# Kernel tuning notes

Measured on AMD Instinct MI355X. Metric: run time of the kernel, lower is better.

Reference implementation:

```python
import jax, jax.numpy as jnp
import numpy as np

QUERY_DIM = 1024
HIDDEN_DIM = 1024


def setup_inputs() -> dict:
    key = jax.random.key(0)
    k1, k2, k3, k4 = jax.random.split(key, 4)
    query = jax.random.normal(k1, (8, 2048, QUERY_DIM), dtype=jnp.float32)
    info = jax.random.normal(k2, (8, 2048, HIDDEN_DIM), dtype=jnp.float32)
    # nn.Linear params: weight [out, in], bias [out]
    bound = 1.0 / np.sqrt(QUERY_DIM)
    W = jax.random.uniform(k3, (HIDDEN_DIM, QUERY_DIM), jnp.float32, -bound, bound)
    b = jax.random.uniform(k4, (HIDDEN_DIM,), jnp.float32, -bound, bound)
    return {"query": query, "info": info, "W": W, "b": b}


def reference(query, info, W, b):
    # Eval mode: dropout is identity.
    # projected query: [B, S, hidden]
    q = jnp.einsum("bsq,hq->bsh", query, W) + b
    # unscaled attention scores over info rows: [B, S, M]
    scores = jax.nn.softmax(jnp.einsum("bsh,bmh->bsm", q, info), axis=-1)
    # weighted sum of info: [B, S, hidden]
    return jnp.einsum("bsm,bmh->bsh", scores, info)
```

## Files before the change

### kernel.cpp

```cpp
#include <hip/hip_runtime.h>

#define DEVI __device__ __forceinline__

typedef __attribute__((ext_vector_type(4))) float f32x4;
typedef __attribute__((ext_vector_type(8))) short bf16x8;

typedef const unsigned __attribute__((address_space(1))) as1_u32;
typedef unsigned __attribute__((address_space(3))) as3_u32;

DEVI unsigned fbits(float x){ union{float f;unsigned u;} v; v.f=x; return v.u; }
DEVI float bitsf(unsigned u){ union{unsigned u;float f;} v; v.u=u; return v.f; }
DEVI short bf_rne(float x){ unsigned u=fbits(x); u += 0x7fffu + ((u>>16)&1u); return (short)(u>>16); }

DEVI unsigned pack_hi2(unsigned u0, unsigned u1){
#if __has_builtin(__builtin_amdgcn_perm)
  return __builtin_amdgcn_perm(u1, u0, 0x07060302u);
#else
  return (u0 >> 16) | (u1 & 0xffff0000u);
#endif
}
DEVI unsigned pack_rne2(float a, float b){
  return (unsigned)(unsigned short)bf_rne(a) | ((unsigned)(unsigned short)bf_rne(b) << 16);
}

DEVI void gload16(const short* g, short* s){
  __builtin_amdgcn_global_load_lds((as1_u32*)g, (as3_u32*)s, 16, 0, 0);
}

__global__ __launch_bounds__(256)
void k_split(const float* __restrict__ in, short* __restrict__ hi,
             short* __restrict__ lo, const long n4)
{
  long i = (long)blockIdx.x*256 + threadIdx.x;
  const long stride = (long)gridDim.x*256;
  for (; i < n4; i += stride){
    const float4 v = ((const float4*)in)[i];
    const unsigned u0=fbits(v.x), u1=fbits(v.y), u2=fbits(v.z), u3=fbits(v.w);
    ((uint2*)hi)[i] = make_uint2(pack_hi2(u0,u1), pack_hi2(u2,u3));
    const float l0 = v.x - bitsf(u0 & 0xffff0000u);
    const float l1 = v.y - bitsf(u1 & 0xffff0000u);
    const float l2 = v.z - bitsf(u2 & 0xffff0000u);
    const float l3 = v.w - bitsf(u3 & 0xffff0000u);
    ((uint2*)lo)[i] = make_uint2(pack_rne2(l0,l1), pack_rne2(l2,l3));
  }
}

template<int NPHASE, bool BIAS, bool SPLIT_OUT>
__global__ __launch_bounds__(256, 2)
void k_gemm(const short* __restrict__ Ah, const short* __restrict__ Al,
            const short* __restrict__ Bh, const short* __restrict__ Bl,
            void* __restrict__ Cv, const float* __restrict__ bias,
            const int K, const int lda, const int ldb, const int ldc,
            const long sAz, const long sBz, const long sCz, const int loOff)
{
  __shared__ short As[128*64];
  __shared__ short Bs[128*64];

  const int tid = threadIdx.x;
  const int w = tid >> 6, l = tid & 63;
  const long bz = blockIdx.z;
  const size_t aOff = (size_t)bz*sAz + (size_t)blockIdx.x*128*lda;
  const size_t bOff = (size_t)bz*sBz + (size_t)blockIdx.y*128*ldb;

  int srow[4], scol[4];
  short *sA[4], *sB[4];
#pragma unroll
  for (int i = 0; i < 4; ++i){
    const int c = w*4 + i;
    const int r = c*8 + (l>>3);
    srow[i] = r;
    scol[i] = ((l&7) ^ (r&7)) << 3;
    sA[i] = As + c*512;
    sB[i] = Bs + c*512;
  }

  const int wr = w >> 1, wc = w & 1;
  const int fr = l & 15, h4 = l >> 4;

  int aoffs[2][4], boffs[2][4];
#pragma unroll
  for (int kk = 0; kk < 2; ++kk)
#pragma unroll
    for (int m = 0; m < 4; ++m){
      const int ra = wr*64 + m*16 + fr;
      aoffs[kk][m] = ra*64 + (((kk*4 + h4) ^ (ra&7)) << 3);
      const int rb = wc*64 + m*16 + fr;
      boffs[kk][m] = rb*64 + (((kk*4 + h4) ^ (rb&7)) << 3);
    }

  f32x4 acc[4][4];
#pragma unroll
  for (int m = 0; m < 4; ++m)
#pragma unroll
    for (int n = 0; n < 4; ++n){ acc[m][n][0]=0.f; acc[m][n][1]=0.f; acc[m][n][2]=0.f; acc[m][n][3]=0.f; }

#pragma unroll 1
  for (int p = 0; p < NPHASE; ++p){
    const short* Ap = ((NPHASE==3 && p==1) ? Al : Ah) + aOff;
    const short* Bp = ((NPHASE==3 && p==2) ? Bl : Bh) + bOff;
#pragma unroll 1
    for (int kt = 0; kt < K; kt += 64){
#pragma unroll
      for (int i = 0; i < 4; ++i){
        gload16(Ap + (size_t)srow[i]*lda + kt + scol[i], sA[i]);
        gload16(Bp + (size_t)srow[i]*ldb + kt + scol[i], sB[i]);
      }
      __syncthreads();
#pragma unroll
      for (int kk = 0; kk < 2; ++kk){
        bf16x8 bfr[4];
#pragma unroll
        for (int n = 0; n < 4; ++n) bfr[n] = *(const bf16x8*)(Bs + boffs[kk][n]);
#pragma unroll
        for (int m = 0; m < 4; ++m){
          const bf16x8 afr = *(const bf16x8*)(As + aoffs[kk][m]);
#pragma unroll
          for (int n = 0; n < 4; ++n)
            acc[m][n] = __builtin_amdgcn_mfma_f32_16x16x32_bf16(afr, bfr[n], acc[m][n], 0,0,0);
        }
      }
      __syncthreads();
    }
  }

  const int rr = h4*4;
  if constexpr (SPLIT_OUT){
    short* Ch = (short*)Cv + (size_t)bz*sCz
              + (size_t)(blockIdx.x*128 + wr*64)*ldc + blockIdx.y*128 + wc*64;
    short* Cl = Ch + loOff;
#pragma unroll
    for (int n = 0; n < 4; ++n){
      const int col = n*16 + fr;
      const float bv = BIAS ? bias[blockIdx.y*128 + wc*64 + col] : 0.f;
#pragma unroll
      for (int m = 0; m < 4; ++m)
#pragma unroll
        for (int j = 0; j < 4; ++j){
          const float v = acc[m][n][j] + bv;
          const unsigned uh = fbits(v) & 0xffff0000u;
          const size_t idx = (size_t)(m*16 + rr + j)*ldc + col;
          Ch[idx] = (short)(uh >> 16);
          Cl[idx] = bf_rne(v - bitsf(uh));
        }
    }
  } else {
    float* C = (float*)Cv + (size_t)bz*sCz
             + (size_t)(blockIdx.x*128 + wr*64)*ldc + blockIdx.y*128 + wc*64;
#pragma unroll
    for (int n = 0; n < 4; ++n){
      const int col = n*16 + fr;
      const float bv = BIAS ? bias[blockIdx.y*128 + wc*64 + col] : 0.f;
#pragma unroll
      for (int m = 0; m < 4; ++m)
#pragma unroll
        for (int j = 0; j < 4; ++j)
          C[(size_t)(m*16 + rr + j)*ldc + col] = acc[m][n][j] + bv;
    }
  }
}

__global__ __launch_bounds__(256)
void k_transpose_bf16(const float* __restrict__ V, short* __restrict__ T,
                      const int MM, const int DD, const long sVz, const long sTz)
{
  __shared__ float t[64][65];
  const float* Vb = V + (long)blockIdx.z*sVz;
  short* Tb = T + (long)blockIdx.z*sTz;
  const int m0 = blockIdx.x*64, d0 = blockIdx.y*64;
  const int tid = threadIdx.x;
#pragma unroll
  for (int i = 0; i < 4; ++i){
    const int c = tid + 256*i;
    const int r = c >> 4, c4 = (c & 15) * 4;
    const float4 v = *(const float4*)(Vb + (size_t)(m0 + r)*DD + d0 + c4);
    t[r][c4+0] = v.x; t[r][c4+1] = v.y; t[r][c4+2] = v.z; t[r][c4+3] = v.w;
  }
  __syncthreads();
#pragma unroll
  for (int i = 0; i < 4; ++i){
    const int c = tid + 256*i;
    const int d = c >> 4, m4 = (c & 15) * 4;
    short4 o;
    o.x = bf_rne(t[m4+0][d]); o.y = bf_rne(t[m4+1][d]);
    o.z = bf_rne(t[m4+2][d]); o.w = bf_rne(t[m4+3][d]);
    *(short4*)(Tb + (size_t)(d0 + d)*MM + m0 + m4) = o;
  }
}

__global__ __launch_bounds__(256)
void k_softmax_rows(float* __restrict__ Sb, const long sz)
{
  float* row = Sb + (long)blockIdx.y*sz + (long)blockIdx.x*2048;
  short* prow = (short*)row;
  const int tid = threadIdx.x;
  const int lane = tid & 63, wid = tid >> 6;

  const float4 v0 = *(const float4*)(row + tid*4);
  const float4 v1 = *(const float4*)(row + 1024 + tid*4);
  float x[8] = {v0.x, v0.y, v0.z, v0.w, v1.x, v1.y, v1.z, v1.w};

  float mx = x[0];
#pragma unroll
  for (int j = 1; j < 8; ++j) mx = fmaxf(mx, x[j]);
#pragma unroll
  for (int off = 32; off; off >>= 1) mx = fmaxf(mx, __shfl_xor(mx, off));

  __shared__ float red[8];
  if (lane == 0) red[wid] = mx;
  __syncthreads();
  mx = fmaxf(fmaxf(red[0], red[1]), fmaxf(red[2], red[3]));

  float e[8]; float s = 0.f;
#pragma unroll
  for (int j = 0; j < 8; ++j){ e[j] = __expf(x[j] - mx); s += e[j]; }
#pragma unroll
  for (int off = 32; off; off >>= 1) s += __shfl_xor(s, off);
  if (lane == 0) red[4 + wid] = s;
  __syncthreads();
  s = (red[4] + red[5]) + (red[6] + red[7]);
  const float inv = 1.0f / s;

  *(uint2*)(prow + tid*4)        = make_uint2(pack_rne2(e[0]*inv, e[1]*inv), pack_rne2(e[2]*inv, e[3]*inv));
  *(uint2*)(prow + 1024 + tid*4) = make_uint2(pack_rne2(e[4]*inv, e[5]*inv), pack_rne2(e[6]*inv, e[7]*inv));
}

extern "C" void kernel_launch(void* const* d_in, const int* in_sizes, int n_in,
                              void* d_out, int out_size, void* d_ws, size_t ws_size,
                              hipStream_t stream)
{
  const float* query = (const float*)d_in[0];
  const float* info  = (const float*)d_in[1];
  const float* Wm    = (const float*)d_in[2];
  const float* bias  = (const float*)d_in[3];
  float* out = (float*)d_out;

  const int B = 8, S = 2048, M = 2048, D = 1024;
  const size_t PB = (size_t)S * D;

  short* info_hi = (short*)d_ws;
  short* info_lo = info_hi + 16777216;
  short* infoT   = info_lo + 16777216;
  short* W_hi    = infoT   + 16777216;
  short* W_lo    = W_hi    + 1048576;
  float* Sbuf    = (float*)(W_lo + 1048576);
  const size_t sb = (size_t)S * M * sizeof(float);
  size_t avail = ws_size > 104857600ull ? ws_size - 104857600ull : 0;
  int nchunk = (int)(avail / sb); if (nchunk > 8) nchunk = 8; if (nchunk < 1) nchunk = 1;

  short* q_s = (short*)d_out;
  const long qBz = 2*(long)PB;
  const int  qLo = (int)PB;

  k_split<<<1024, 256, 0, stream>>>(Wm, W_hi, W_lo, (long)(D*D/4));

  int nb = 2*nchunk; if (nb > 8) nb = 8;
  for (int q0 = 0; q0 < B; q0 += nb){
    const int cur = (q0 + nb <= B) ? nb : (B - q0);
    short* qt_hi = (short*)Sbuf;
    short* qt_lo = qt_hi + (size_t)cur*PB;
    k_split<<<2048, 256, 0, stream>>>(query + (size_t)q0*PB, qt_hi, qt_lo,
                                      (long)((size_t)cur*PB/4));
    k_gemm<3, true, true><<<dim3(S/128, D/128, cur), 256, 0, stream>>>(
        qt_hi, qt_lo, W_hi, W_lo, q_s + (size_t)q0*qBz, bias,
        D, D, D, D, (long)PB, 0L, qBz, qLo);
  }

  k_split<<<2048, 256, 0, stream>>>(info, info_hi, info_lo, (long)(B*PB/4));
  k_transpose_bf16<<<dim3(M/64, D/64, B), 256, 0, stream>>>(
      info, infoT, M, D, (long)PB, (long)PB);

  for (int b0 = 0; b0 < B; b0 += nchunk){
    const int cur = (b0 + nchunk <= B) ? nchunk : (B - b0);

    const short* qh = q_s + (size_t)b0*qBz;
    k_gemm<3, false, false><<<dim3(S/128, M/128, cur), 256, 0, stream>>>(
        qh, qh + qLo, info_hi + (size_t)b0*PB, info_lo + (size_t)b0*PB,
        Sbuf, nullptr, D, D, D, M, qBz, (long)PB, (long)S*M, 0);

    k_softmax_rows<<<dim3(S, cur), 256, 0, stream>>>(Sbuf, (long)S*M);

    k_gemm<1, false, false><<<dim3(S/128, D/128, cur), 256, 0, stream>>>(
        (const short*)Sbuf, nullptr, infoT + (size_t)b0*PB, nullptr,
        out + (size_t)b0*PB, nullptr, M, 2*M, M, D,
        (long)(2*(size_t)S*M), (long)PB, (long)PB, 0);
  }
}
```

Baseline: 538.0 us.

## Rewrite GEMM as 256x256 double-buffered pipelined tile and fuse info prep

The bf16 MFMA GEMM moves from a 128x128 tile with 256 threads and synchronous single-buffer loads to a 256x256 tile with 512 threads. It double-buffers in 128KB of LDS, interleaves global-to-LDS prefetch with MFMA phases using explicit waitcnt, sched barriers and setprio, and swizzles the workgroup order for L2 locality. The info split and the transpose are fused into one kernel so info is read once. The larger tile raises data reuse and hides load latency, at the cost of heavy register pressure (128 accumulators per lane), fewer workgroups and fragile hand-tuned waitcnt ordering.

```diff
diff --git a/kernel.cpp b/kernel.cpp
--- a/kernel.cpp
+++ b/kernel.cpp
@@ -26,6 +26,16 @@
 DEVI void gload16(const short* g, short* s){
   __builtin_amdgcn_global_load_lds((as1_u32*)g, (as3_u32*)s, 16, 0, 0);
 }
+
+#define SBAR() { __builtin_amdgcn_sched_barrier(0); asm volatile("" ::: "memory"); \
+                 __builtin_amdgcn_s_barrier(); __builtin_amdgcn_sched_barrier(0); }
+
+#define MF(a,b,c) __builtin_amdgcn_mfma_f32_16x16x32_bf16(a,b,c,0,0,0)
+#define MROW(M, x) \
+  acc[M][0] = MF(x, bb0, acc[M][0]); \
+  acc[M][1] = MF(x, bb1, acc[M][1]); \
+  acc[M][2] = MF(x, bb2, acc[M][2]); \
+  acc[M][3] = MF(x, bb3, acc[M][3]);
 
 __global__ __launch_bounds__(256)
 void k_split(const float* __restrict__ in, short* __restrict__ hi,
@@ -46,94 +56,168 @@
 }
 
 template<int NPHASE, bool BIAS, bool SPLIT_OUT>
-__global__ __launch_bounds__(256, 2)
+__global__ __launch_bounds__(512, 2)
 void k_gemm(const short* __restrict__ Ah, const short* __restrict__ Al,
             const short* __restrict__ Bh, const short* __restrict__ Bl,
             void* __restrict__ Cv, const float* __restrict__ bias,
             const int K, const int lda, const int ldb, const int ldc,
             const long sAz, const long sBz, const long sCz, const int loOff)
 {
-  __shared__ short As[128*64];
-  __shared__ short Bs[128*64];
+  __shared__ short LDS[65536];
 
   const int tid = threadIdx.x;
   const int w = tid >> 6, l = tid & 63;
+  const int wr = w >> 2, wc = w & 3;
+  const int fr = l & 15, h4 = l >> 4;
   const long bz = blockIdx.z;
-  const size_t aOff = (size_t)bz*sAz + (size_t)blockIdx.x*128*lda;
-  const size_t bOff = (size_t)bz*sBz + (size_t)blockIdx.y*128*ldb;
-
-  int srow[4], scol[4];
-  short *sA[4], *sB[4];
-#pragma unroll
-  for (int i = 0; i < 4; ++i){
-    const int c = w*4 + i;
-    const int r = c*8 + (l>>3);
-    srow[i] = r;
-    scol[i] = ((l&7) ^ (r&7)) << 3;
-    sA[i] = As + c*512;
-    sB[i] = Bs + c*512;
-  }
-
-  const int wr = w >> 1, wc = w & 1;
-  const int fr = l & 15, h4 = l >> 4;
-
-  int aoffs[2][4], boffs[2][4];
-#pragma unroll
-  for (int kk = 0; kk < 2; ++kk)
-#pragma unroll
-    for (int m = 0; m < 4; ++m){
-      const int ra = wr*64 + m*16 + fr;
-      aoffs[kk][m] = ra*64 + (((kk*4 + h4) ^ (ra&7)) << 3);
-      const int rb = wc*64 + m*16 + fr;
-      boffs[kk][m] = rb*64 + (((kk*4 + h4) ^ (rb&7)) << 3);
-    }
-
-  f32x4 acc[4][4];
-#pragma unroll
-  for (int m = 0; m < 4; ++m)
+
+  const int nwg = gridDim.x * gridDim.y;
+  const int xy  = blockIdx.y * gridDim.x + blockIdx.x;
+  const int q8  = nwg >> 3;
+  const int sw  = (xy & 7) * q8 + (xy >> 3);
+  const int bx  = sw % gridDim.x;
+  const int by  = sw / gridDim.x;
+
+  const size_t aOff = (size_t)bz*sAz + (size_t)bx*256*lda;
+  const size_t bOff = (size_t)bz*sBz + (size_t)by*256*ldb;
+
+  const int sch = (((l & 7) ^ ((l >> 3) & 7)) << 3);
+  const int rA0 = wr*128 + (w & 3)*8 + (l >> 3);
+  int aoffg[4];
+#pragma unroll
+  for (int q2 = 0; q2 < 4; ++q2) aoffg[q2] = (rA0 + 32*q2)*lda;
+  const int rB0 = wc*64 + (w >> 2)*8 + (l >> 3);
+  int boffg[4];
+#pragma unroll
+  for (int j2 = 0; j2 < 4; ++j2) boffg[j2] = (rB0 + 16*j2)*ldb;
+  const int dAu = wr*8192 + (w & 3)*512;
+  const int dBu = 16384 + wc*4096 + (w >> 2)*512;
+
+  const int rbA = (wr*128 + fr)*64;
+  const int rbB = 16384 + (wc*64 + fr)*64;
+  const int c08 = ((h4     ) ^ (l & 7)) << 3;
+  const int c18 = ((h4 + 4 ) ^ (l & 7)) << 3;
+
+  f32x4 acc[8][4];
+#pragma unroll
+  for (int m = 0; m < 8; ++m)
 #pragma unroll
     for (int n = 0; n < 4; ++n){ acc[m][n][0]=0.f; acc[m][n][1]=0.f; acc[m][n][2]=0.f; acc[m][n][3]=0.f; }
 
+  const short* Asrc = Ah + aOff + sch;
+  const short* Bsrc = Bh + bOff + sch;
+  int skt = 0, spass = 0;
+  const int nkt = NPHASE * (K >> 6);
+
+  {
+    short* dB0 = LDS + dBu;
+    short* dA0 = LDS + dAu;
+    gload16(Bsrc + boffg[0], dB0);
+    gload16(Bsrc + boffg[1], dB0 + 1024);
+    gload16(Bsrc + boffg[2], dB0 + 2048);
+    gload16(Bsrc + boffg[3], dB0 + 3072);
+    gload16(Asrc + aoffg[0], dA0);
+    gload16(Asrc + aoffg[1], dA0 + 2048);
+    gload16(Asrc + aoffg[2], dA0 + 4096);
+    gload16(Asrc + aoffg[3], dA0 + 6144);
+  }
+  skt = 64; Asrc += 64; Bsrc += 64;
+  asm volatile("s_waitcnt vmcnt(2)" ::: "memory");
+  SBAR();
+
+#define ADVANCE()                                                            \
+  { skt += 64;                                                               \
+    if (skt == K){ skt = 0; ++spass;                                         \
+      Asrc = ((NPHASE==3 && spass==1) ? Al : Ah) + aOff + sch;               \
+      Bsrc = ((NPHASE==3 && spass==2) ? Bl : Bh) + bOff + sch;               \
+    } else { Asrc += 64; Bsrc += 64; } }
+
+#define TILE(CO, PF, VA, VB)                                                 \
+{                                                                            \
+  const short* pA = LDS + (CO) + rbA;                                        \
+  const short* pB = LDS + (CO) + rbB;                                        \
+  short* dAp = LDS + ((CO)^32768) + dAu;                                     \
+  short* dBp = LDS + ((CO)^32768) + dBu;                                     \
+  bf16x8 aA,aB,aC,aD, bb0,bb1,bb2,bb3;                                       \
+                                            \
+  if (PF){ gload16(Bsrc + boffg[0], dBp); gload16(Bsrc + boffg[1], dBp + 1024); } \
+  bb0 = *(const bf16x8*)(pB +        c08);                                   \
+  bb1 = *(const bf16x8*)(pB + 1024 + c08);                                   \
+  bb2 = *(const bf16x8*)(pB + 2048 + c08);                                   \
+  bb3 = *(const bf16x8*)(pB + 3072 + c08);                                   \
+  aA  = *(const bf16x8*)(pA +        c08);                                   \
+  aB  = *(const bf16x8*)(pA + 1024 + c08);                                   \
+  aC  = *(const bf16x8*)(pA + 2048 + c08);                                   \
+  aD  = *(const bf16x8*)(pA + 3072 + c08);                                   \
+  SBAR();                                                                    \
+  __builtin_amdgcn_s_setprio(1);                                             \
+  MROW(0,aA) MROW(1,aB) MROW(2,aC) MROW(3,aD)                                \
+  __builtin_amdgcn_s_setprio(0);                                             \
+  asm volatile("s_waitcnt vmcnt(" VA ")" ::: "memory");                      \
+  SBAR();                                                                    \
+                                                    \
+  if (PF){ gload16(Bsrc + boffg[2], dBp + 2048); gload16(Bsrc + boffg[3], dBp + 3072); } \
+  aA = *(const bf16x8*)(pA + 4096 + c08);                                    \
+  aB = *(const bf16x8*)(pA + 5120 + c08);                                    \
+  aC = *(const bf16x8*)(pA + 6144 + c08);                                    \
+  aD = *(const bf16x8*)(pA + 7168 + c08);                                    \
+  SBAR();                                                                    \
+  __builtin_amdgcn_s_setprio(1);                                             \
+  MROW(4,aA) MROW(5,aB) MROW(6,aC) MROW(7,aD)                                \
+  __builtin_amdgcn_s_setprio(0);                                             \
+  SBAR();                                                                    \
+                                            \
+  if (PF){ gload16(Asrc + aoffg[0], dAp); gload16(Asrc + aoffg[1], dAp + 2048); } \
+  bb0 = *(const bf16x8*)(pB +        c18);                                   \
+  bb1 = *(const bf16x8*)(pB + 1024 + c18);                                   \
+  bb2 = *(const bf16x8*)(pB + 2048 + c18);                                   \
+  bb3 = *(const bf16x8*)(pB + 3072 + c18);                                   \
+  aA  = *(const bf16x8*)(pA +        c18);                                   \
+  aB  = *(const bf16x8*)(pA + 1024 + c18);                                   \
+  aC  = *(const bf16x8*)(pA + 2048 + c18);                                   \
+  aD  = *(const bf16x8*)(pA + 3072 + c18);                                   \
+  SBAR();                                                                    \
+  __builtin_amdgcn_s_setprio(1);                                             \
+  MROW(0,aA) MROW(1,aB) MROW(2,aC) MROW(3,aD)                                \
+  __builtin_amdgcn_s_setprio(0);                                             \
+  SBAR();                                                                    \
+                                                    \
+  if (PF){ gload16(Asrc + aoffg[2], dAp + 4096); gload16(Asrc + aoffg[3], dAp + 6144); } \
+  aA = *(const bf16x8*)(pA + 4096 + c18);                                    \
+  aB = *(const bf16x8*)(pA + 5120 + c18);                                    \
+  aC = *(const bf16x8*)(pA + 6144 + c18);                                    \
+  aD = *(const bf16x8*)(pA + 7168 + c18);                                    \
+  SBAR();                                                                    \
+  __builtin_amdgcn_s_setprio(1);                                             \
+  MROW(4,aA) MROW(5,aB) MROW(6,aC) MROW(7,aD)                                \
+  __builtin_amdgcn_s_setprio(0);                                             \
+  if (PF){ ADVANCE(); }                                                      \
+  asm volatile("s_waitcnt vmcnt(" VB ")" ::: "memory");                      \
+  SBAR();                                                                    \
+}
+
 #pragma unroll 1
-  for (int p = 0; p < NPHASE; ++p){
-    const short* Ap = ((NPHASE==3 && p==1) ? Al : Ah) + aOff;
-    const short* Bp = ((NPHASE==3 && p==2) ? Bl : Bh) + bOff;
-#pragma unroll 1
-    for (int kt = 0; kt < K; kt += 64){
-#pragma unroll
-      for (int i = 0; i < 4; ++i){
-        gload16(Ap + (size_t)srow[i]*lda + kt + scol[i], sA[i]);
-        gload16(Bp + (size_t)srow[i]*ldb + kt + scol[i], sB[i]);
-      }
-      __syncthreads();
-#pragma unroll
-      for (int kk = 0; kk < 2; ++kk){
-        bf16x8 bfr[4];
-#pragma unroll
-        for (int n = 0; n < 4; ++n) bfr[n] = *(const bf16x8*)(Bs + boffs[kk][n]);
-#pragma unroll
-        for (int m = 0; m < 4; ++m){
-          const bf16x8 afr = *(const bf16x8*)(As + aoffs[kk][m]);
-#pragma unroll
-          for (int n = 0; n < 4; ++n)
-            acc[m][n] = __builtin_amdgcn_mfma_f32_16x16x32_bf16(afr, bfr[n], acc[m][n], 0,0,0);
-        }
-      }
-      __syncthreads();
-    }
-  }
+  for (int it = 0; it < nkt - 2; it += 2){
+    TILE(0,     1, "2", "2")
+    TILE(32768, 1, "2", "2")
+  }
+  TILE(0,     1, "2", "2")
+  TILE(32768, 0, "0", "0")
+
+#undef TILE
+#undef ADVANCE
 
   const int rr = h4*4;
   if constexpr (SPLIT_OUT){
     short* Ch = (short*)Cv + (size_t)bz*sCz
-              + (size_t)(blockIdx.x*128 + wr*64)*ldc + blockIdx.y*128 + wc*64;
+              + (size_t)(bx*256 + wr*128)*ldc + by*256 + wc*64;
     short* Cl = Ch + loOff;
 #pragma unroll
     for (int n = 0; n < 4; ++n){
       const int col = n*16 + fr;
-      const float bv = BIAS ? bias[blockIdx.y*128 + wc*64 + col] : 0.f;
-#pragma unroll
-      for (int m = 0; m < 4; ++m)
+      const float bv = BIAS ? bias[by*256 + wc*64 + col] : 0.f;
+#pragma unroll
+      for (int m = 0; m < 8; ++m)
 #pragma unroll
         for (int j = 0; j < 4; ++j){
           const float v = acc[m][n][j] + bv;
@@ -145,13 +229,13 @@
     }
   } else {
     float* C = (float*)Cv + (size_t)bz*sCz
-             + (size_t)(blockIdx.x*128 + wr*64)*ldc + blockIdx.y*128 + wc*64;
+             + (size_t)(bx*256 + wr*128)*ldc + by*256 + wc*64;
 #pragma unroll
     for (int n = 0; n < 4; ++n){
       const int col = n*16 + fr;
-      const float bv = BIAS ? bias[blockIdx.y*128 + wc*64 + col] : 0.f;
-#pragma unroll
-      for (int m = 0; m < 4; ++m)
+      const float bv = BIAS ? bias[by*256 + wc*64 + col] : 0.f;
+#pragma unroll
+      for (int m = 0; m < 8; ++m)
 #pragma unroll
         for (int j = 0; j < 4; ++j)
           C[(size_t)(m*16 + rr + j)*ldc + col] = acc[m][n][j] + bv;
@@ -160,26 +244,37 @@
 }
 
 __global__ __launch_bounds__(256)
-void k_transpose_bf16(const float* __restrict__ V, short* __restrict__ T,
-                      const int MM, const int DD, const long sVz, const long sTz)
+void k_prep_info(const float* __restrict__ V, short* __restrict__ hi,
+                 short* __restrict__ lo, short* __restrict__ T,
+                 const int MM, const int DD, const long sVz, const long sTz)
 {
   __shared__ float t[64][65];
   const float* Vb = V + (long)blockIdx.z*sVz;
-  short* Tb = T + (long)blockIdx.z*sTz;
+  short* hb = hi + (long)blockIdx.z*sVz;
+  short* lb = lo + (long)blockIdx.z*sVz;
+  short* Tb = T  + (long)blockIdx.z*sTz;
   const int m0 = blockIdx.x*64, d0 = blockIdx.y*64;
   const int tid = threadIdx.x;
 #pragma unroll
   for (int i = 0; i < 4; ++i){
     const int c = tid + 256*i;
-    const int r = c >> 4, c4 = (c & 15) * 4;
+    const int r = c >> 4, c4 = (c & 15)*4;
     const float4 v = *(const float4*)(Vb + (size_t)(m0 + r)*DD + d0 + c4);
-    t[r][c4+0] = v.x; t[r][c4+1] = v.y; t[r][c4+2] = v.z; t[r][c4+3] = v.w;
+    t[r][c4+0]=v.x; t[r][c4+1]=v.y; t[r][c4+2]=v.z; t[r][c4+3]=v.w;
+    const unsigned u0=fbits(v.x), u1=fbits(v.y), u2=fbits(v.z), u3=fbits(v.w);
+    const size_t gi = (size_t)(m0 + r)*DD + d0 + c4;
+    *(uint2*)(hb + gi) = make_uint2(pack_hi2(u0,u1), pack_hi2(u2,u3));
+    const float l0 = v.x - bitsf(u0 & 0xffff0000u);
+    const float l1 = v.y - bitsf(u1 & 0xffff0000u);
+    const float l2 = v.z - bitsf(u2 & 0xffff0000u);
+    const float l3 = v.w - bitsf(u3 & 0xffff0000u);
+    *(uint2*)(lb + gi) = make_uint2(pack_rne2(l0,l1), pack_rne2(l2,l3));
   }
   __syncthreads();
 #pragma unroll
   for (int i = 0; i < 4; ++i){
     const int c = tid + 256*i;
-    const int d = c >> 4, m4 = (c & 15) * 4;
+    const int d = c >> 4, m4 = (c & 15)*4;
     short4 o;
     o.x = bf_rne(t[m4+0][d]); o.y = bf_rne(t[m4+1][d]);
     o.z = bf_rne(t[m4+2][d]); o.w = bf_rne(t[m4+3][d]);
@@ -260,26 +355,25 @@
     short* qt_lo = qt_hi + (size_t)cur*PB;
     k_split<<<2048, 256, 0, stream>>>(query + (size_t)q0*PB, qt_hi, qt_lo,
                                       (long)((size_t)cur*PB/4));
-    k_gemm<3, true, true><<<dim3(S/128, D/128, cur), 256, 0, stream>>>(
+    k_gemm<3, true, true><<<dim3(S/256, D/256, cur), 512, 0, stream>>>(
         qt_hi, qt_lo, W_hi, W_lo, q_s + (size_t)q0*qBz, bias,
         D, D, D, D, (long)PB, 0L, qBz, qLo);
   }
 
-  k_split<<<2048, 256, 0, stream>>>(info, info_hi, info_lo, (long)(B*PB/4));
-  k_transpose_bf16<<<dim3(M/64, D/64, B), 256, 0, stream>>>(
-      info, infoT, M, D, (long)PB, (long)PB);
+  k_prep_info<<<dim3(M/64, D/64, B), 256, 0, stream>>>(
+      info, info_hi, info_lo, infoT, M, D, (long)PB, (long)PB);
 
   for (int b0 = 0; b0 < B; b0 += nchunk){
     const int cur = (b0 + nchunk <= B) ? nchunk : (B - b0);
 
     const short* qh = q_s + (size_t)b0*qBz;
-    k_gemm<3, false, false><<<dim3(S/128, M/128, cur), 256, 0, stream>>>(
+    k_gemm<3, false, false><<<dim3(S/256, M/256, cur), 512, 0, stream>>>(
         qh, qh + qLo, info_hi + (size_t)b0*PB, info_lo + (size_t)b0*PB,
         Sbuf, nullptr, D, D, D, M, qBz, (long)PB, (long)S*M, 0);
 
     k_softmax_rows<<<dim3(S, cur), 256, 0, stream>>>(Sbuf, (long)S*M);
 
-    k_gemm<1, false, false><<<dim3(S/128, D/128, cur), 256, 0, stream>>>(
+    k_gemm<1, false, false><<<dim3(S/256, D/256, cur), 512, 0, stream>>>(
         (const short*)Sbuf, nullptr, infoT + (size_t)b0*PB, nullptr,
         out + (size_t)b0*PB, nullptr, M, 2*M, M, D,
         (long)(2*(size_t)S*M), (long)PB, (long)PB, 0);
```

Result: faster. 450.6 us (-16.2%).
